# Kernel optimization log

Measured on AMD Instinct MI355X. Metric: run time of the kernel, lower is better.

Reference implementation:

```python
import jax, jax.numpy as jnp
import numpy as np

STRIDES = (8, 16, 32, 64, 128)
IMG = 1024
NUM_CLS = 80
SHRINK_RATIO = 0.2
BIG = 1e7  # padding value for area of non-positive locations (matches tf.pad constant)


def _level_targets(boxes, labels, valid, stride):
    """Vectorized per-level target assignment.
    boxes: [B,M,4] float, labels: [B,M] int32, valid: [B,M] bool.
    Replaces the per-box tf.map_fn + dynamic pad + argmin + gather_nd with a
    dense masked area map and a single argmin/gather pass.
    """
    B, M, _ = boxes.shape
    fh = fw = IMG // stride
    HW = fh * fw
    # shrink_and_normalize_boxes: scale to level, shrink around center, clamp
    b = boxes / stride
    cx = (b[..., 0] + b[..., 2]) * 0.5
    cy = (b[..., 1] + b[..., 3]) * 0.5
    hw = (b[..., 2] - b[..., 0]) * 0.5 * SHRINK_RATIO
    hh = (b[..., 3] - b[..., 1]) * 0.5 * SHRINK_RATIO
    px1 = jnp.maximum(jnp.floor(cx - hw), 0.0)
    py1 = jnp.maximum(jnp.floor(cy - hh), 0.0)
    px2 = jnp.minimum(jnp.ceil(cx + hw), float(fw))
    py2 = jnp.minimum(jnp.ceil(cy + hh), float(fh))
    xs = jnp.arange(fw, dtype=jnp.float32)
    ys = jnp.arange(fh, dtype=jnp.float32)
    in_x = (xs[None, None, None, :] >= px1[:, :, None, None]) & (xs[None, None, None, :] < px2[:, :, None, None])
    in_y = (ys[None, None, :, None] >= py1[:, :, None, None]) & (ys[None, None, :, None] < py2[:, :, None, None])
    inside = in_x & in_y & valid[:, :, None, None]  # [B,M,fh,fw]
    area = (boxes[..., 2] - boxes[..., 0]) * (boxes[..., 3] - boxes[..., 1])  # [B,M]
    area_map = jnp.where(inside, area[:, :, None, None], BIG)  # [B,M,fh,fw]
    winner = jnp.argmin(area_map, axis=1).reshape(B, HW)  # min-area box per pixel
    win_area = jnp.min(area_map, axis=1).reshape(B, HW)
    pos = win_area < BIG  # pixel covered by at least one valid box
    posf = pos.astype(jnp.float32)
    wb = jnp.take_along_axis(boxes, winner[..., None], axis=1)  # [B,HW,4]
    wl = jnp.take_along_axis(labels, winner, axis=1)            # [B,HW]
    yy, xx = jnp.meshgrid(ys, xs, indexing='ij')
    sx = (xx.reshape(-1) + 0.5) * stride  # [HW] anchor-point x in image coords
    sy = (yy.reshape(-1) + 0.5) * stride
    l = sx[None, :] - wb[..., 0]
    t = sy[None, :] - wb[..., 1]
    r = wb[..., 2] - sx[None, :]
    btm = wb[..., 3] - sy[None, :]
    reg = jnp.stack([l, t, r, btm], axis=-1) / (4.0 * stride)  # [B,HW,4]
    eps = 1e-6
    cent = jnp.sqrt(
        jnp.clip(jnp.minimum(l, r) / jnp.maximum(jnp.maximum(l, r), eps), 0.0, 1.0)
        * jnp.clip(jnp.minimum(t, btm) / jnp.maximum(jnp.maximum(t, btm), eps), 0.0, 1.0))
    soft = jnp.where(pos, cent, 1.0)  # negatives padded with 1 (constant_values=1)
    cls_onehot = jax.nn.one_hot(wl, NUM_CLS, dtype=jnp.float32) * posf[..., None]
    cls_t = jnp.concatenate([cls_onehot, soft[..., None], posf[..., None]], axis=-1)  # [B,HW,C+2]
    reg_t = jnp.concatenate([reg * posf[..., None], soft[..., None], posf[..., None]], axis=-1)  # [B,HW,6]
    ind = jnp.where(pos, winner, -1).astype(jnp.int32)
    return cls_t, reg_t, ind


def setup_inputs():
    key = jax.random.key(0)
    B, M = 16, 100
    k1, k2, k3, k4, k5, k6 = jax.random.split(key, 6)
    w = jax.random.uniform(k1, (B, M)) * 240.0 + 16.0
    h = jax.random.uniform(k2, (B, M)) * 240.0 + 16.0
    cx = jax.random.uniform(k3, (B, M)) * (IMG - 260.0) + 130.0
    cy = jax.random.uniform(k4, (B, M)) * (IMG - 260.0) + 130.0
    labels = jax.random.randint(k5, (B, M), 0, NUM_CLS).astype(jnp.float32)
    x1 = cx - w * 0.5
    x2 = cx + w * 0.5
    y1 = cy - h * 0.5
    y2 = cy + h * 0.5
    # zero-pad trailing boxes per batch element (trim_zero_padding_boxes convention)
    n_valid = jax.random.randint(k6, (B,), 10, M + 1)
    valid = jnp.arange(M)[None, :] < n_valid[:, None]
    gt_boxes = jnp.stack([x1, y1, x2, y2, labels], axis=-1) * valid[..., None]
    return {"gt_boxes": gt_boxes.astype(jnp.float32)}


def reference(gt_boxes):
    boxes = gt_boxes[..., :4]
    labels = gt_boxes[..., 4].astype(jnp.int32)
    valid = jnp.sum(jnp.abs(boxes), axis=-1) > 0.0  # trim_zero_padding_boxes
    cls_all, reg_all, ind_all = [], [], []
    for stride in STRIDES:  # fixed 5 FPN levels
        c, r, i = _level_targets(boxes, labels, valid, stride)
        cls_all.append(c)
        reg_all.append(r)
        ind_all.append(i)
    cls_t = jnp.concatenate(cls_all, axis=1)   # [B, 21824, 82]
    reg_t = jnp.concatenate(reg_all, axis=1)   # [B, 21824, 6]
    ind_t = jnp.concatenate(ind_all, axis=1)[..., None]  # [B, 21824, 1]
    num_boxes = jnp.sum(valid.astype(jnp.int32), axis=1, keepdims=True)  # [B,1]
    return cls_t, reg_t, ind_t, num_boxes
```

## Files before the change

kernel.cpp:

```cpp
#include <hip/hip_runtime.h>
#include <stdint.h>

#define NCLS   80
#define HWTOT  21824
#define MBOX   100

#define REG_OFF 28633088ull
#define IND_OFF 30728192ull
#define NB_OFF  31077376ull

__global__ __launch_bounds__(256)
void sapd_targets(const float* __restrict__ gt, float* __restrict__ out)
{
    const int tid = threadIdx.x;
    const int c   = blockIdx.x;
    const int b   = blockIdx.y;

    int lvl, pix0, base;
    if      (c < 64) { lvl = 0; pix0 = c << 8;        base = 0;     }
    else if (c < 80) { lvl = 1; pix0 = (c - 64) << 8; base = 16384; }
    else if (c < 84) { lvl = 2; pix0 = (c - 80) << 8; base = 20480; }
    else if (c < 85) { lvl = 3; pix0 = 0;             base = 21504; }
    else             { lvl = 4; pix0 = 0;             base = 21760; }

    const int   l2fw   = 7 - lvl;
    const int   fw     = 1 << l2fw;
    const float fs     = (float)(8 << lvl);
    const int   chunkN = (lvl == 4) ? 64 : 256;

    const size_t rowbase = (size_t)b * HWTOT + base + pix0;

    __shared__ float4   sBox[MBOX];
    __shared__ int      sLab[MBOX];
    __shared__ float2   sCull[MBOX];
    __shared__ int      sOrig[MBOX];
    __shared__ int      sN;
    __shared__ float2   sSP[256];
    __shared__ float    rReg[256 * 4];

    {
        float4* o4 = (float4*)(out + rowbase * 82);
        const int n4 = (chunkN * 82) >> 2;
        const float4 z = make_float4(0.0f, 0.0f, 0.0f, 0.0f);
        for (int i = tid; i < n4; i += 256) o4[i] = z;
    }

    if (tid < 64) {
        const int lane = tid;
        const int ry0 = pix0 >> l2fw;
        const int ry1 = ry0 + (chunkN >> l2fw);
        int n0 = 0;
        int nvalid = 0;
        #pragma unroll
        for (int h = 0; h < 2; ++h) {
            const int m = h * 64 + lane;
            bool pred = false;
            bool valid = false;
            uint32_t bb = 0;
            float area = 0.0f;
            if (m < MBOX) {
                const float* g = gt + ((size_t)b * MBOX + m) * 5;
                float x1 = g[0], y1 = g[1], x2 = g[2], y2 = g[3], lab = g[4];
                valid = (fabsf(x1) + fabsf(y1) + fabsf(x2) + fabsf(y2)) > 0.0f;
                area  = (x2 - x1) * (y2 - y1);
                float bx1 = x1 / fs, by1 = y1 / fs, bx2 = x2 / fs, by2 = y2 / fs;
                float cx = (bx1 + bx2) * 0.5f, cy = (by1 + by2) * 0.5f;
                float hw = (bx2 - bx1) * 0.5f * 0.2f, hh = (by2 - by1) * 0.5f * 0.2f;
                float px1 = fmaxf(floorf(cx - hw), 0.0f);
                float py1 = fmaxf(floorf(cy - hh), 0.0f);
                float px2 = fminf(ceilf(cx + hw), (float)fw);
                float py2 = fminf(ceilf(cy + hh), (float)fw);
                int ix1 = (int)px1, iy1 = (int)py1, ix2 = (int)px2, iy2 = (int)py2;
                bb = (uint32_t)ix1 | ((uint32_t)iy1 << 8) |
                     ((uint32_t)ix2 << 16) | ((uint32_t)iy2 << 24);
                pred = valid && (ix2 > ix1) && (iy2 > ry0) && (iy1 < ry1);
                sBox[m] = make_float4(x1, y1, x2, y2);
                sLab[m] = (int)lab;
            }
            unsigned long long mk = __ballot(pred);
            unsigned long long vk = __ballot(valid);
            if (pred) {
                int p = n0 + __popcll(mk & ((1ull << lane) - 1ull));
                sCull[p] = make_float2(__uint_as_float(bb), area);
                sOrig[p] = m;
            }
            n0 += __popcll(mk);
            nvalid += __popcll(vk);
        }
        if (lane == 0) {
            sN = n0;
            if (lvl == 4) out[NB_OFF + b] = (float)nvalid;
        }
    }
    __syncthreads();

    float soft = 1.0f, posf = 0.0f;
    int   tgtcol = 0, posflag = 0;
    if (tid < chunkN) {
        const int p  = pix0 + tid;
        const int px = p & (fw - 1);
        const int py = p >> l2fw;
        float bestA = 1e30f; int bestI = -1;
        const int n = sN;
        for (int i = 0; i < n; ++i) {
            float2 e = sCull[i];
            uint32_t bb = __float_as_uint(e.x);
            int x1 = bb & 255, y1 = (bb >> 8) & 255, x2 = (bb >> 16) & 255, y2 = bb >> 24;
            bool hit = (px >= x1) & (px < x2) & (py >= y1) & (py < y2);
            bool upd = hit & (e.y < bestA);
            bestA = upd ? e.y : bestA;
            bestI = upd ? i : bestI;
        }
        bool pos = bestI >= 0;
        int orig = pos ? sOrig[bestI] : 0;
        float4 bx = sBox[orig];
        float sx = ((float)px + 0.5f) * fs;
        float sy = ((float)py + 0.5f) * fs;
        float l  = sx - bx.x, t = sy - bx.y, r = bx.z - sx, bt = bx.w - sy;
        float inv4s = 1.0f / (4.0f * fs);
        posf = pos ? 1.0f : 0.0f;
        const float eps = 1e-6f;
        float a1 = fminf(l, r) / fmaxf(fmaxf(l, r), eps);
        a1 = fminf(fmaxf(a1, 0.0f), 1.0f);
        float a2 = fminf(t, bt) / fmaxf(fmaxf(t, bt), eps);
        a2 = fminf(fmaxf(a2, 0.0f), 1.0f);
        float cent = sqrtf(a1 * a2);
        soft = pos ? cent : 1.0f;
        tgtcol  = pos ? sLab[orig] : 0;
        posflag = pos ? 1 : 0;
        sSP[tid] = make_float2(soft, posf);
        rReg[tid * 4 + 0] = l  * inv4s * posf;
        rReg[tid * 4 + 1] = t  * inv4s * posf;
        rReg[tid * 4 + 2] = r  * inv4s * posf;
        rReg[tid * 4 + 3] = bt * inv4s * posf;
        out[IND_OFF + rowbase + tid] = pos ? (float)orig : -1.0f;
    }

    __syncthreads();

    if (tid < chunkN) {
        const size_t row0 = (rowbase + (size_t)tid) * 82ull;
        *(float2*)(out + row0 + 80) = make_float2(soft, posf);
        if (posflag) out[row0 + tgtcol] = 1.0f;
    }

    {
        float4* o4 = (float4*)(out + REG_OFF + rowbase * 6);
        const int n4 = (chunkN * 6) >> 2;
        for (int i = tid; i < n4; i += 256) {
            int idx = i << 2;
            float v[4];
            #pragma unroll
            for (int k = 0; k < 4; ++k) {
                int id  = idx + k;
                int row = (int)((unsigned)id / 6u);
                int col = id - row * 6;
                float2 m = sSP[row];
                v[k] = (col < 4) ? rReg[row * 4 + col] : ((col == 4) ? m.x : m.y);
            }
            o4[i] = make_float4(v[0], v[1], v[2], v[3]);
        }
    }
}

extern "C" void kernel_launch(void* const* d_in, const int* in_sizes, int n_in,
                              void* d_out, int out_size, void* d_ws, size_t ws_size,
                              hipStream_t stream)
{
    const float* gt = (const float*)d_in[0];
    float* out = (float*)d_out;
    sapd_targets<<<dim3(86, 16), 256, 0, stream>>>(gt, out);
}
```

Baseline: 131.7 us.

## Warp-specialize: one wavefront does culling and matching while others zero-fill

Splits the block so the first wavefront handles box culling plus the per-pixel min-area search, with each lane covering four pixels. The other three wavefronts zero the class rows at the same time. This removes one block barrier and lets the global zero-fill overlap with the matching compute. The cost is that the matching loop now runs on a single wavefront, with four accumulators per lane, instead of on up to four wavefronts in parallel.

Result: slower. 136.0 us (+3.2%).

```diff
diff --git a/kernel.cpp b/kernel.cpp
--- a/kernel.cpp
+++ b/kernel.cpp
@@ -34,18 +34,16 @@
     __shared__ int      sLab[MBOX];
     __shared__ float2   sCull[MBOX];
     __shared__ int      sOrig[MBOX];
-    __shared__ int      sN;
     __shared__ float2   sSP[256];
+    __shared__ int      sTgt[256];
     __shared__ float    rReg[256 * 4];
 
-    {
+    if (tid >= 64) {
         float4* o4 = (float4*)(out + rowbase * 82);
         const int n4 = (chunkN * 82) >> 2;
         const float4 z = make_float4(0.0f, 0.0f, 0.0f, 0.0f);
-        for (int i = tid; i < n4; i += 256) o4[i] = z;
-    }
-
-    if (tid < 64) {
+        for (int i = tid - 64; i < n4; i += 192) o4[i] = z;
+    } else {
         const int lane = tid;
         const int ry0 = pix0 >> l2fw;
         const int ry1 = ry0 + (chunkN >> l2fw);
@@ -54,8 +52,7 @@
         #pragma unroll
         for (int h = 0; h < 2; ++h) {
             const int m = h * 64 + lane;
-            bool pred = false;
-            bool valid = false;
+            bool pred = false, valid = false;
             uint32_t bb = 0;
             float area = 0.0f;
             if (m < MBOX) {
@@ -84,64 +81,71 @@
                 sCull[p] = make_float2(__uint_as_float(bb), area);
                 sOrig[p] = m;
             }
-            n0 += __popcll(mk);
+            n0     += __popcll(mk);
             nvalid += __popcll(vk);
         }
-        if (lane == 0) {
-            sN = n0;
-            if (lvl == 4) out[NB_OFF + b] = (float)nvalid;
+        if (lvl == 4 && lane == 0) out[NB_OFF + b] = (float)nvalid;
+
+        int px_[4], py_[4];
+        float bestA[4];
+        int   bestI[4];
+        #pragma unroll
+        for (int j = 0; j < 4; ++j) {
+            int p = pix0 + lane + j * 64;
+            px_[j] = p & (fw - 1);
+            py_[j] = p >> l2fw;
+            bestA[j] = 1e30f;
+            bestI[j] = -1;
         }
-    }
-    __syncthreads();
-
-    float soft = 1.0f, posf = 0.0f;
-    int   tgtcol = 0, posflag = 0;
-    if (tid < chunkN) {
-        const int p  = pix0 + tid;
-        const int px = p & (fw - 1);
-        const int py = p >> l2fw;
-        float bestA = 1e30f; int bestI = -1;
-        const int n = sN;
-        for (int i = 0; i < n; ++i) {
+        for (int i = 0; i < n0; ++i) {
             float2 e = sCull[i];
             uint32_t bb = __float_as_uint(e.x);
             int x1 = bb & 255, y1 = (bb >> 8) & 255, x2 = (bb >> 16) & 255, y2 = bb >> 24;
-            bool hit = (px >= x1) & (px < x2) & (py >= y1) & (py < y2);
-            bool upd = hit & (e.y < bestA);
-            bestA = upd ? e.y : bestA;
-            bestI = upd ? i : bestI;
+            #pragma unroll
+            for (int j = 0; j < 4; ++j) {
+                bool hit = (px_[j] >= x1) & (px_[j] < x2) & (py_[j] >= y1) & (py_[j] < y2);
+                bool upd = hit & (e.y < bestA[j]);
+                bestA[j] = upd ? e.y : bestA[j];
+                bestI[j] = upd ? i  : bestI[j];
+            }
         }
-        bool pos = bestI >= 0;
-        int orig = pos ? sOrig[bestI] : 0;
-        float4 bx = sBox[orig];
-        float sx = ((float)px + 0.5f) * fs;
-        float sy = ((float)py + 0.5f) * fs;
-        float l  = sx - bx.x, t = sy - bx.y, r = bx.z - sx, bt = bx.w - sy;
-        float inv4s = 1.0f / (4.0f * fs);
-        posf = pos ? 1.0f : 0.0f;
-        const float eps = 1e-6f;
-        float a1 = fminf(l, r) / fmaxf(fmaxf(l, r), eps);
-        a1 = fminf(fmaxf(a1, 0.0f), 1.0f);
-        float a2 = fminf(t, bt) / fmaxf(fmaxf(t, bt), eps);
-        a2 = fminf(fmaxf(a2, 0.0f), 1.0f);
-        float cent = sqrtf(a1 * a2);
-        soft = pos ? cent : 1.0f;
-        tgtcol  = pos ? sLab[orig] : 0;
-        posflag = pos ? 1 : 0;
-        sSP[tid] = make_float2(soft, posf);
-        rReg[tid * 4 + 0] = l  * inv4s * posf;
-        rReg[tid * 4 + 1] = t  * inv4s * posf;
-        rReg[tid * 4 + 2] = r  * inv4s * posf;
-        rReg[tid * 4 + 3] = bt * inv4s * posf;
-        out[IND_OFF + rowbase + tid] = pos ? (float)orig : -1.0f;
+        #pragma unroll
+        for (int j = 0; j < 4; ++j) {
+            const int row = lane + j * 64;
+            bool pos = bestI[j] >= 0;
+            int orig = pos ? sOrig[bestI[j]] : 0;
+            float4 bx = sBox[orig];
+            float sx = ((float)px_[j] + 0.5f) * fs;
+            float sy = ((float)py_[j] + 0.5f) * fs;
+            float l  = sx - bx.x, t = sy - bx.y, r = bx.z - sx, bt = bx.w - sy;
+            float inv4s = 1.0f / (4.0f * fs);
+            float posf  = pos ? 1.0f : 0.0f;
+            const float eps = 1e-6f;
+            float a1 = fminf(l, r) / fmaxf(fmaxf(l, r), eps);
+            a1 = fminf(fmaxf(a1, 0.0f), 1.0f);
+            float a2 = fminf(t, bt) / fmaxf(fmaxf(t, bt), eps);
+            a2 = fminf(fmaxf(a2, 0.0f), 1.0f);
+            float cent = sqrtf(a1 * a2);
+            float soft = pos ? cent : 1.0f;
+            sSP[row]  = make_float2(soft, posf);
+            sTgt[row] = pos ? sLab[orig] : -1;
+            rReg[row * 4 + 0] = l  * inv4s * posf;
+            rReg[row * 4 + 1] = t  * inv4s * posf;
+            rReg[row * 4 + 2] = r  * inv4s * posf;
+            rReg[row * 4 + 3] = bt * inv4s * posf;
+            if (row < chunkN)
+                out[IND_OFF + rowbase + row] = pos ? (float)orig : -1.0f;
+        }
     }
 
     __syncthreads();
 
     if (tid < chunkN) {
+        float2 sp = sSP[tid];
         const size_t row0 = (rowbase + (size_t)tid) * 82ull;
-        *(float2*)(out + row0 + 80) = make_float2(soft, posf);
-        if (posflag) out[row0 + tgtcol] = 1.0f;
+        *(float2*)(out + row0 + 80) = sp;
+        int tg = sTgt[tid];
+        if (tg >= 0) out[row0 + tg] = 1.0f;
     }
 
     {
```

## Make each wavefront independent to eliminate block-wide barriers

Applied to the files above, without the earlier changes.

Every 64-lane wavefront now loads the boxes, culls them against its own 64-pixel span (including an x-range test), and keeps private LDS copies. This removes both __syncthreads and the serialization where one wave did the culling while the others waited. The zeroing of the class rows is also per-wave, and the regression output is staged in LDS as contiguous 6-float rows so it can be copied out directly. The cost is four times the redundant box preprocessing and more LDS use, plus an explicit vmcnt wait that makes the class-row scatter land after the zeroing.

After: 127.2 us. 3.4% less time.

```diff
diff --git a/kernel.cpp b/kernel.cpp
--- a/kernel.cpp
+++ b/kernel.cpp
@@ -12,9 +12,11 @@
 __global__ __launch_bounds__(256)
 void sapd_targets(const float* __restrict__ gt, float* __restrict__ out)
 {
-    const int tid = threadIdx.x;
-    const int c   = blockIdx.x;
-    const int b   = blockIdx.y;
+    const int tid  = threadIdx.x;
+    const int w    = tid >> 6;
+    const int lane = tid & 63;
+    const int c    = blockIdx.x;
+    const int b    = blockIdx.y;
 
     int lvl, pix0, base;
     if      (c < 64) { lvl = 0; pix0 = c << 8;        base = 0;     }
@@ -28,138 +30,152 @@
     const float fs     = (float)(8 << lvl);
     const int   chunkN = (lvl == 4) ? 64 : 256;
 
+    if (w * 64 >= chunkN) return;
+
     const size_t rowbase = (size_t)b * HWTOT + base + pix0;
+    const int    row     = w * 64 + lane;
+    const int    p0      = pix0 + w * 64;
 
-    __shared__ float4   sBox[MBOX];
-    __shared__ int      sLab[MBOX];
-    __shared__ float2   sCull[MBOX];
-    __shared__ int      sOrig[MBOX];
-    __shared__ int      sN;
-    __shared__ float2   sSP[256];
-    __shared__ float    rReg[256 * 4];
+    __shared__ float2 sCull[4][MBOX];
+    __shared__ int    sOrig[4][MBOX];
+    __shared__ float4 sBox [4][MBOX];
+    __shared__ int    sLab [4][MBOX];
+    __shared__ float  sReg [4][64 * 6];
+
+    const int ry0 = p0 >> l2fw;
+    const int ry1 = ((p0 + 63) >> l2fw) + 1;
+    int pxlo, pxhi;
+    if (fw >= 64) { pxlo = p0 & (fw - 1); pxhi = pxlo + 63; }
+    else          { pxlo = 0;             pxhi = fw - 1;    }
+
+    const float* g0 = gt + ((size_t)b * MBOX + lane) * 5;
+    float ax1 = g0[0], ay1 = g0[1], ax2 = g0[2], ay2 = g0[3], alab = g0[4];
+    const int  mb   = 64 + lane;
+    const bool hasb = mb < MBOX;
+    float bx1 = 0, by1 = 0, bx2 = 0, by2 = 0, blab = 0;
+    if (hasb) {
+        const float* g1 = gt + ((size_t)b * MBOX + mb) * 5;
+        bx1 = g1[0]; by1 = g1[1]; bx2 = g1[2]; by2 = g1[3]; blab = g1[4];
+    }
+
+    int nW = 0, nvalid = 0;
+    {
+        bool valid = (fabsf(ax1) + fabsf(ay1) + fabsf(ax2) + fabsf(ay2)) > 0.0f;
+        float area = (ax2 - ax1) * (ay2 - ay1);
+        float q1 = ax1 / fs, q2 = ay1 / fs, q3 = ax2 / fs, q4 = ay2 / fs;
+        float cx = (q1 + q3) * 0.5f, cy = (q2 + q4) * 0.5f;
+        float hw = (q3 - q1) * 0.5f * 0.2f, hh = (q4 - q2) * 0.5f * 0.2f;
+        int ix1 = (int)fmaxf(floorf(cx - hw), 0.0f);
+        int iy1 = (int)fmaxf(floorf(cy - hh), 0.0f);
+        int ix2 = (int)fminf(ceilf(cx + hw), (float)fw);
+        int iy2 = (int)fminf(ceilf(cy + hh), (float)fw);
+        uint32_t bb = (uint32_t)ix1 | ((uint32_t)iy1 << 8) |
+                      ((uint32_t)ix2 << 16) | ((uint32_t)iy2 << 24);
+        bool pred = valid && (ix2 > ix1) && (iy2 > ry0) && (iy1 < ry1)
+                          && (ix1 <= pxhi) && (ix2 > pxlo);
+        sBox[w][lane] = make_float4(ax1, ay1, ax2, ay2);
+        sLab[w][lane] = (int)alab;
+        unsigned long long mk = __ballot(pred);
+        nvalid += __popcll(__ballot(valid));
+        if (pred) {
+            int pp = __popcll(mk & ((1ull << lane) - 1ull));
+            sCull[w][pp] = make_float2(__uint_as_float(bb), area);
+            sOrig[w][pp] = lane;
+        }
+        nW += __popcll(mk);
+    }
+    {
+        bool valid = false, pred = false;
+        uint32_t bb = 0;
+        float area = 0.0f;
+        if (hasb) {
+            valid = (fabsf(bx1) + fabsf(by1) + fabsf(bx2) + fabsf(by2)) > 0.0f;
+            area  = (bx2 - bx1) * (by2 - by1);
+            float q1 = bx1 / fs, q2 = by1 / fs, q3 = bx2 / fs, q4 = by2 / fs;
+            float cx = (q1 + q3) * 0.5f, cy = (q2 + q4) * 0.5f;
+            float hw = (q3 - q1) * 0.5f * 0.2f, hh = (q4 - q2) * 0.5f * 0.2f;
+            int ix1 = (int)fmaxf(floorf(cx - hw), 0.0f);
+            int iy1 = (int)fmaxf(floorf(cy - hh), 0.0f);
+            int ix2 = (int)fminf(ceilf(cx + hw), (float)fw);
+            int iy2 = (int)fminf(ceilf(cy + hh), (float)fw);
+            bb = (uint32_t)ix1 | ((uint32_t)iy1 << 8) |
+                 ((uint32_t)ix2 << 16) | ((uint32_t)iy2 << 24);
+            pred = valid && (ix2 > ix1) && (iy2 > ry0) && (iy1 < ry1)
+                         && (ix1 <= pxhi) && (ix2 > pxlo);
+            sBox[w][mb] = make_float4(bx1, by1, bx2, by2);
+            sLab[w][mb] = (int)blab;
+        }
+        unsigned long long mk = __ballot(pred);
+        nvalid += __popcll(__ballot(valid));
+        if (pred) {
+            int pp = nW + __popcll(mk & ((1ull << lane) - 1ull));
+            sCull[w][pp] = make_float2(__uint_as_float(bb), area);
+            sOrig[w][pp] = mb;
+        }
+        nW += __popcll(mk);
+    }
+    if (lvl == 4 && lane == 0) out[NB_OFF + b] = (float)nvalid;
+
+    __builtin_amdgcn_sched_barrier(0);
+    {
+        float4* o4 = (float4*)(out + (rowbase + (size_t)(w * 64)) * 82ull);
+        const float4 z = make_float4(0.0f, 0.0f, 0.0f, 0.0f);
+        for (int i = lane; i < 1312; i += 64) o4[i] = z;
+    }
+    __builtin_amdgcn_sched_barrier(0);
+
+    const int px = (pix0 + row) & (fw - 1);
+    const int py = (pix0 + row) >> l2fw;
+    float bestA = 1e30f; int bestI = -1;
+    for (int i = 0; i < nW; ++i) {
+        float2 e = sCull[w][i];
+        uint32_t bbv = __float_as_uint(e.x);
+        int x1 = bbv & 255, y1 = (bbv >> 8) & 255, x2 = (bbv >> 16) & 255, y2 = bbv >> 24;
+        bool hit = (px >= x1) & (px < x2) & (py >= y1) & (py < y2);
+        bool upd = hit & (e.y < bestA);
+        bestA = upd ? e.y : bestA;
+        bestI = upd ? i : bestI;
+    }
+
+    bool pos  = bestI >= 0;
+    int  orig = pos ? sOrig[w][bestI] : 0;
+    float4 bx = sBox[w][orig];
+    float sx = ((float)px + 0.5f) * fs;
+    float sy = ((float)py + 0.5f) * fs;
+    float l  = sx - bx.x, t = sy - bx.y, r = bx.z - sx, bt = bx.w - sy;
+    float inv4s = 1.0f / (4.0f * fs);
+    float posf  = pos ? 1.0f : 0.0f;
+    const float eps = 1e-6f;
+    float a1 = fminf(l, r) / fmaxf(fmaxf(l, r), eps);
+    a1 = fminf(fmaxf(a1, 0.0f), 1.0f);
+    float a2 = fminf(t, bt) / fmaxf(fmaxf(t, bt), eps);
+    a2 = fminf(fmaxf(a2, 0.0f), 1.0f);
+    float cent = sqrtf(a1 * a2);
+    float soft = pos ? cent : 1.0f;
+    int   tgt  = pos ? sLab[w][orig] : -1;
+    {
+        float* rr = &sReg[w][lane * 6];
+        rr[0] = l  * inv4s * posf;
+        rr[1] = t  * inv4s * posf;
+        rr[2] = r  * inv4s * posf;
+        rr[3] = bt * inv4s * posf;
+        rr[4] = soft;
+        rr[5] = posf;
+    }
+    out[IND_OFF + rowbase + row] = pos ? (float)orig : -1.0f;
+
+    asm volatile("s_waitcnt vmcnt(0)" ::: "memory");
 
     {
-        float4* o4 = (float4*)(out + rowbase * 82);
-        const int n4 = (chunkN * 82) >> 2;
-        const float4 z = make_float4(0.0f, 0.0f, 0.0f, 0.0f);
-        for (int i = tid; i < n4; i += 256) o4[i] = z;
-    }
-
-    if (tid < 64) {
-        const int lane = tid;
-        const int ry0 = pix0 >> l2fw;
-        const int ry1 = ry0 + (chunkN >> l2fw);
-        int n0 = 0;
-        int nvalid = 0;
-        #pragma unroll
-        for (int h = 0; h < 2; ++h) {
-            const int m = h * 64 + lane;
-            bool pred = false;
-            bool valid = false;
-            uint32_t bb = 0;
-            float area = 0.0f;
-            if (m < MBOX) {
-                const float* g = gt + ((size_t)b * MBOX + m) * 5;
-                float x1 = g[0], y1 = g[1], x2 = g[2], y2 = g[3], lab = g[4];
-                valid = (fabsf(x1) + fabsf(y1) + fabsf(x2) + fabsf(y2)) > 0.0f;
-                area  = (x2 - x1) * (y2 - y1);
-                float bx1 = x1 / fs, by1 = y1 / fs, bx2 = x2 / fs, by2 = y2 / fs;
-                float cx = (bx1 + bx2) * 0.5f, cy = (by1 + by2) * 0.5f;
-                float hw = (bx2 - bx1) * 0.5f * 0.2f, hh = (by2 - by1) * 0.5f * 0.2f;
-                float px1 = fmaxf(floorf(cx - hw), 0.0f);
-                float py1 = fmaxf(floorf(cy - hh), 0.0f);
-                float px2 = fminf(ceilf(cx + hw), (float)fw);
-                float py2 = fminf(ceilf(cy + hh), (float)fw);
-                int ix1 = (int)px1, iy1 = (int)py1, ix2 = (int)px2, iy2 = (int)py2;
-                bb = (uint32_t)ix1 | ((uint32_t)iy1 << 8) |
-                     ((uint32_t)ix2 << 16) | ((uint32_t)iy2 << 24);
-                pred = valid && (ix2 > ix1) && (iy2 > ry0) && (iy1 < ry1);
-                sBox[m] = make_float4(x1, y1, x2, y2);
-                sLab[m] = (int)lab;
-            }
-            unsigned long long mk = __ballot(pred);
-            unsigned long long vk = __ballot(valid);
-            if (pred) {
-                int p = n0 + __popcll(mk & ((1ull << lane) - 1ull));
-                sCull[p] = make_float2(__uint_as_float(bb), area);
-                sOrig[p] = m;
-            }
-            n0 += __popcll(mk);
-            nvalid += __popcll(vk);
-        }
-        if (lane == 0) {
-            sN = n0;
-            if (lvl == 4) out[NB_OFF + b] = (float)nvalid;
-        }
-    }
-    __syncthreads();
-
-    float soft = 1.0f, posf = 0.0f;
-    int   tgtcol = 0, posflag = 0;
-    if (tid < chunkN) {
-        const int p  = pix0 + tid;
-        const int px = p & (fw - 1);
-        const int py = p >> l2fw;
-        float bestA = 1e30f; int bestI = -1;
-        const int n = sN;
-        for (int i = 0; i < n; ++i) {
-            float2 e = sCull[i];
-            uint32_t bb = __float_as_uint(e.x);
-            int x1 = bb & 255, y1 = (bb >> 8) & 255, x2 = (bb >> 16) & 255, y2 = bb >> 24;
-            bool hit = (px >= x1) & (px < x2) & (py >= y1) & (py < y2);
-            bool upd = hit & (e.y < bestA);
-            bestA = upd ? e.y : bestA;
-            bestI = upd ? i : bestI;
-        }
-        bool pos = bestI >= 0;
-        int orig = pos ? sOrig[bestI] : 0;
-        float4 bx = sBox[orig];
-        float sx = ((float)px + 0.5f) * fs;
-        float sy = ((float)py + 0.5f) * fs;
-        float l  = sx - bx.x, t = sy - bx.y, r = bx.z - sx, bt = bx.w - sy;
-        float inv4s = 1.0f / (4.0f * fs);
-        posf = pos ? 1.0f : 0.0f;
-        const float eps = 1e-6f;
-        float a1 = fminf(l, r) / fmaxf(fmaxf(l, r), eps);
-        a1 = fminf(fmaxf(a1, 0.0f), 1.0f);
-        float a2 = fminf(t, bt) / fmaxf(fmaxf(t, bt), eps);
-        a2 = fminf(fmaxf(a2, 0.0f), 1.0f);
-        float cent = sqrtf(a1 * a2);
-        soft = pos ? cent : 1.0f;
-        tgtcol  = pos ? sLab[orig] : 0;
-        posflag = pos ? 1 : 0;
-        sSP[tid] = make_float2(soft, posf);
-        rReg[tid * 4 + 0] = l  * inv4s * posf;
-        rReg[tid * 4 + 1] = t  * inv4s * posf;
-        rReg[tid * 4 + 2] = r  * inv4s * posf;
-        rReg[tid * 4 + 3] = bt * inv4s * posf;
-        out[IND_OFF + rowbase + tid] = pos ? (float)orig : -1.0f;
-    }
-
-    __syncthreads();
-
-    if (tid < chunkN) {
-        const size_t row0 = (rowbase + (size_t)tid) * 82ull;
+        const size_t row0 = (rowbase + (size_t)row) * 82ull;
         *(float2*)(out + row0 + 80) = make_float2(soft, posf);
-        if (posflag) out[row0 + tgtcol] = 1.0f;
+        if (tgt >= 0) out[row0 + tgt] = 1.0f;
     }
 
     {
-        float4* o4 = (float4*)(out + REG_OFF + rowbase * 6);
-        const int n4 = (chunkN * 6) >> 2;
-        for (int i = tid; i < n4; i += 256) {
-            int idx = i << 2;
-            float v[4];
-            #pragma unroll
-            for (int k = 0; k < 4; ++k) {
-                int id  = idx + k;
-                int row = (int)((unsigned)id / 6u);
-                int col = id - row * 6;
-                float2 m = sSP[row];
-                v[k] = (col < 4) ? rReg[row * 4 + col] : ((col == 4) ? m.x : m.y);
-            }
-            o4[i] = make_float4(v[0], v[1], v[2], v[3]);
-        }
+        float4* o4 = (float4*)(out + REG_OFF + (rowbase + (size_t)(w * 64)) * 6ull);
+        const float4* s4 = (const float4*)&sReg[w][0];
+        for (int i = lane; i < 96; i += 64) o4[i] = s4[i];
     }
 }
 
```
